# Optimization experiments

Hardware: AMD Instinct MI355X
Metric: run time of the kernel (lower is better)

Reference implementation:

```python
import jax, jax.numpy as jnp
import numpy as np

B, NQ, NKV = 16, 4096, 77
QUERY_DIM, CONTEXT_DIM = 320, 768
HEADS, DIM_HEAD = 8, 64
INNER = HEADS * DIM_HEAD
SCALE = DIM_HEAD ** (-0.5)
MAX_NEG = -jnp.finfo(jnp.float32).max / 2


def setup_inputs() -> dict:
    key = jax.random.key(0)
    ks = jax.random.split(key, 8)
    x = jax.random.normal(ks[0], (B, NQ, QUERY_DIM), dtype=jnp.float32)
    context = jax.random.normal(ks[1], (B, NKV, CONTEXT_DIM), dtype=jnp.float32)
    mask = jax.random.randint(ks[2], (B, 1, 1, NKV), 0, 2).astype(bool)
    s = 0.02
    Wq = jax.random.normal(ks[3], (QUERY_DIM, INNER), dtype=jnp.float32) * s
    Wk = jax.random.normal(ks[4], (CONTEXT_DIM, INNER), dtype=jnp.float32) * s
    Wv = jax.random.normal(ks[5], (CONTEXT_DIM, INNER), dtype=jnp.float32) * s
    Wo = jax.random.normal(ks[6], (INNER, QUERY_DIM), dtype=jnp.float32) * s
    bo = jnp.zeros((QUERY_DIM,), dtype=jnp.float32)
    return {"x": x, "context": context, "mask": mask,
            "Wq": Wq, "Wk": Wk, "Wv": Wv, "Wo": Wo, "bo": bo}


def reference(x, context, mask, Wq, Wk, Wv, Wo, bo):
    # projections (bias-free Linears)
    q = (x @ Wq).reshape(B, NQ, HEADS, DIM_HEAD)        # b q h d
    k = (context @ Wk).reshape(B, NKV, HEADS, DIM_HEAD)  # b k h d
    v = (context @ Wv).reshape(B, NKV, HEADS, DIM_HEAD)  # b k h d
    # additive mask bias: 0 where mask, -finfo.max/2 where ~mask (matches masked_fill_)
    bias = jnp.where(mask, jnp.float32(0), MAX_NEG)      # broadcast to b h q k
    sim = jnp.einsum('bqhd,bkhd->bhqk', q, k) * SCALE + bias
    attn = jax.nn.softmax(sim, axis=-1)
    out = jnp.einsum('bhqk,bkhd->bqhd', attn, v).reshape(B, NQ, INNER)
    return out @ Wo + bo  # dropout p=0 -> identity
```

## Files before the change

### kernel.cpp

```cpp
#include <hip/hip_runtime.h>

typedef unsigned short ushort_t;
typedef __attribute__((ext_vector_type(8))) short bf16x8;
typedef __attribute__((ext_vector_type(4))) float f32x4;

#define B_SZ   16
#define NQ     4096
#define NKV    77
#define QDIM   320
#define CDIM   768
#define HEADS  8
#define DHEAD  64
#define INNER  512
#define M_ROWS (B_SZ * NQ)
#define VT_STR 104

__device__ __forceinline__ ushort_t f2bf(float f) {
  unsigned u = __builtin_bit_cast(unsigned, f);
  u = (u + 0x7fffu + ((u >> 16) & 1u)) >> 16;
  return (ushort_t)u;
}

__device__ __forceinline__ void async16(const ushort_t* g, ushort_t* l) {
  __builtin_amdgcn_global_load_lds(
      (const __attribute__((address_space(1))) unsigned int*)g,
      (__attribute__((address_space(3))) unsigned int*)l,
      16, 0, 0);
}

#define VMCNT(N) asm volatile("s_waitcnt vmcnt(" #N ")" ::: "memory")

#define PREP_X  5242880
#define PREP_T0 (PREP_X + 236544)
#define PREP_T1 (PREP_T0 + 163840)
#define PREP_T2 (PREP_T1 + 786432)
#define PREP_T3 (PREP_T2 + 196608)
__global__ void prep_kernel(const float* __restrict__ x, ushort_t* __restrict__ xb,
                            const float* __restrict__ ctx, ushort_t* __restrict__ cb,
                            const float* __restrict__ Wq, ushort_t* __restrict__ Wqb,
                            const float* __restrict__ Wk, const float* __restrict__ Wv,
                            ushort_t* __restrict__ Wkvb,
                            const float* __restrict__ Wo, ushort_t* __restrict__ Wob,
                            const unsigned char* __restrict__ mraw,
                            float* __restrict__ biasT) {
  if (blockIdx.x == 0) {
    __shared__ int s_u8, s_w4;
    if (threadIdx.x == 0) { s_u8 = 0; s_w4 = 0; }
    __syncthreads();
    const int nbytes = B_SZ * NKV;
    for (int i = threadIdx.x; i < nbytes; i += blockDim.x) {
      unsigned char v = mraw[i];
      if (v && (i & 3)) atomicOr(&s_u8, 1);
      if (v && ((i & 7) == 4)) atomicOr(&s_w4, 1);
    }
    __syncthreads();
    int mode = s_u8 ? 0 : (s_w4 ? 1 : 2);
    for (int i = threadIdx.x; i < B_SZ * 80; i += blockDim.x) {
      int b = i / 80, kv = i - b * 80;
      float bias = -2e30f;
      if (kv < NKV) {
        int idx = b * NKV + kv;
        long long m;
        if (mode == 0)      m = (long long)mraw[idx];
        else if (mode == 1) m = (long long)((const int*)mraw)[idx];
        else                m = ((const long long*)mraw)[idx];
        bias = m ? 0.0f : -1e30f;
      }
      biasT[i] = bias;
    }
  }
  int i = blockIdx.x * blockDim.x + threadIdx.x;
  const int stride = gridDim.x * blockDim.x;
  for (; i < PREP_T3; i += stride) {
    if (i < PREP_X) {
      float4 v = ((const float4*)x)[i];
      ushort4 o;
      o.x = f2bf(v.x); o.y = f2bf(v.y); o.z = f2bf(v.z); o.w = f2bf(v.w);
      ((ushort4*)xb)[i] = o;
    } else if (i < PREP_T0) {
      int j = i - PREP_X;
      float4 v = ((const float4*)ctx)[j];
      ushort4 o;
      o.x = f2bf(v.x); o.y = f2bf(v.y); o.z = f2bf(v.z); o.w = f2bf(v.w);
      ((ushort4*)cb)[j] = o;
    } else if (i < PREP_T1) {
      int j = i - PREP_T0;
      int n = j / QDIM, k = j - n * QDIM;
      Wqb[j] = f2bf(Wq[(size_t)k * INNER + n] * 0.125f);
    } else if (i < PREP_T2) {
      int j = i - PREP_T1;
      int n = j / CDIM, k = j - n * CDIM;
      float v = (n < INNER) ? Wk[(size_t)k * INNER + n]
                            : Wv[(size_t)k * INNER + (n - INNER)];
      Wkvb[j] = f2bf(v);
    } else {
      int j = i - PREP_T2;
      int n = j / INNER, k = j - n * INNER;
      Wob[j] = (n < QDIM) ? f2bf(Wo[(size_t)k * QDIM + n]) : (ushort_t)0;
    }
  }
}

__global__ __launch_bounds__(256) void gemm_bf16(
    const ushort_t* __restrict__ A, const ushort_t* __restrict__ Bt,
    ushort_t* __restrict__ Cb,
    int K, int Astride, int Bstride, int Cstride) {
  __shared__ ushort_t As[128 * 64];
  __shared__ ushort_t Bs[128 * 64];
  const int tid = threadIdx.x;
  const int wid = tid >> 6, lane = tid & 63;
  const int wr = wid >> 1, wc = wid & 1;
  const int tileM = blockIdx.x * 128, tileN = blockIdx.y * 128;

  f32x4 acc[4][4];
#pragma unroll
  for (int m = 0; m < 4; ++m)
#pragma unroll
    for (int n = 0; n < 4; ++n) acc[m][n] = (f32x4){0.f, 0.f, 0.f, 0.f};

  const int srow = lane >> 3;
  const int scol = (lane & 7) * 8;

  for (int kt = 0; kt < K; kt += 64) {
    __syncthreads();
#pragma unroll
    for (int j = 0; j < 4; ++j) {
      int s = wid * 4 + j;
      const ushort_t* ga = A + (size_t)(tileM + s * 8 + srow) * Astride + kt + scol;
      const ushort_t* gb = Bt + (size_t)(tileN + s * 8 + srow) * Bstride + kt + scol;
      async16(ga, As + s * 512);
      async16(gb, Bs + s * 512);
    }
    __syncthreads();
#pragma unroll
    for (int kc = 0; kc < 2; ++kc) {
      bf16x8 af[4], bfr[4];
#pragma unroll
      for (int m = 0; m < 4; ++m)
        af[m] = *(const bf16x8*)&As[(wr * 64 + m * 16 + (lane & 15)) * 64 + kc * 32 + (lane >> 4) * 8];
#pragma unroll
      for (int n = 0; n < 4; ++n)
        bfr[n] = *(const bf16x8*)&Bs[(wc * 64 + n * 16 + (lane & 15)) * 64 + kc * 32 + (lane >> 4) * 8];
#pragma unroll
      for (int m = 0; m < 4; ++m)
#pragma unroll
        for (int n = 0; n < 4; ++n)
          acc[m][n] = __builtin_amdgcn_mfma_f32_16x16x32_bf16(af[m], bfr[n], acc[m][n], 0, 0, 0);
    }
  }

  const int r0 = tileM + wr * 64;
  const int c0 = tileN + wc * 64;
  const int rl2 = (lane >> 4) * 4;
  const int cl = lane & 15;
#pragma unroll
  for (int m = 0; m < 4; ++m)
#pragma unroll
    for (int n = 0; n < 4; ++n) {
      int col = c0 + n * 16 + cl;
#pragma unroll
      for (int r = 0; r < 4; ++r)
        Cb[(size_t)(r0 + m * 16 + rl2 + r) * Cstride + col] = f2bf(acc[m][n][r]);
    }
}

__global__ void vtrans_kernel(const ushort_t* __restrict__ kvb,
                              ushort_t* __restrict__ vt) {
  const int h = blockIdx.y, b = blockIdx.z;
  const int wid = threadIdx.x >> 6, lane = threadIdx.x & 63;
  const int d = blockIdx.x * 4 + wid;
  ushort_t* dst = vt + (size_t)(b * HEADS + h) * (64 * VT_STR) + d * VT_STR;
  for (int kv = lane; kv < VT_STR; kv += 64)
    dst[kv] = (kv < NKV)
        ? kvb[(size_t)(b * NKV + kv) * 1024 + 512 + h * 64 + d]
        : (ushort_t)0;
}

__global__ __launch_bounds__(512, 2) void gemm_qproj_o(
    const ushort_t* __restrict__ A, const ushort_t* __restrict__ Wt,
    ushort_t* __restrict__ qb) {
  extern __shared__ char sm[];
  const int tid = threadIdx.x, wid = tid >> 6, lane = tid & 63;
  const int rl = lane & 15, g = lane >> 4;
  const int wr = wid & 1, wc = wid >> 1;
  const size_t Mbase = (size_t)blockIdx.x * 128;

  size_t asrc; unsigned adst;
  {
    int c = tid, row = c >> 2, c16 = c & 3;
    asrc = (Mbase + row) * 640 + (unsigned)((c16 * 16) ^ ((row & 3) << 4));
    adst = c * 16;
  }
  size_t bsrc[4]; unsigned bdst[4];
#pragma unroll
  for (int i = 0; i < 4; ++i) {
    int c = tid + i * 512, row = c >> 2, c16 = c & 3;
    bsrc[i] = (size_t)row * 640 + (unsigned)((c16 * 16) ^ ((row & 3) << 4));
    bdst[i] = 8192 + c * 16;
  }
  const char* AB = (const char*)A;
  const char* WtB = (const char*)Wt;

  f32x4 acc[4][8];
#pragma unroll
  for (int m = 0; m < 4; ++m)
#pragma unroll
    for (int n = 0; n < 8; ++n) acc[m][n] = (f32x4){0.f, 0.f, 0.f, 0.f};

#define QSTAGE2(K)                                                          \
  {                                                                         \
    char* bb = sm + (unsigned)((K) % 3) * 40960u;                           \
    async16((const ushort_t*)(AB + asrc + (size_t)(K) * 64),                \
            (ushort_t*)(bb + adst));                                        \
    _Pragma("unroll")                                                       \
    for (int i = 0; i < 4; ++i)                                             \
      async16((const ushort_t*)(WtB + bsrc[i] + (size_t)(K) * 64),          \
              (ushort_t*)(bb + bdst[i]));                                   \
  }

  QSTAGE2(0)
  QSTAGE2(1)
  for (int s = 0; s < 10; ++s) {
    if (s < 8) QSTAGE2(s + 2)
    if (s < 8)       { VMCNT(10); }
    else if (s == 8) { VMCNT(5); }
    else             { VMCNT(0); }
    __builtin_amdgcn_sched_barrier(0);
    __builtin_amdgcn_s_barrier();
    __builtin_amdgcn_sched_barrier(0);

    const char* Ab = sm + (unsigned)(s % 3) * 40960u;
    const char* Bb = Ab + 8192;
    bf16x8 af[4], bfr[8];
#pragma unroll
    for (int m = 0; m < 4; ++m) {
      const int row = wr * 64 + m * 16 + rl;
      af[m] = *(const bf16x8*)(Ab + row * 64 + ((g * 16) ^ ((row & 3) << 4)));
    }
#pragma unroll
    for (int n = 0; n < 8; ++n) {
      const int row = wc * 128 + n * 16 + rl;
      bfr[n] = *(const bf16x8*)(Bb + row * 64 + ((g * 16) ^ ((row & 3) << 4)));
    }
#pragma unroll
    for (int m = 0; m < 4; ++m)
#pragma unroll
      for (int n = 0; n < 8; ++n)
        acc[m][n] = __builtin_amdgcn_mfma_f32_16x16x32_bf16(af[m], bfr[n], acc[m][n], 0, 0, 0);
    __builtin_amdgcn_sched_barrier(0);
    __builtin_amdgcn_s_barrier();
    __builtin_amdgcn_sched_barrier(0);
  }

  ushort_t* eb = (ushort_t*)sm;
#pragma unroll
  for (int h = 0; h < 2; ++h) {
    if (h) __syncthreads();
    if (wr == h) {
#pragma unroll
      for (int m = 0; m < 4; ++m)
#pragma unroll
        for (int n = 0; n < 8; ++n)
#pragma unroll
          for (int r = 0; r < 4; ++r)
            eb[(m * 16 + g * 4 + r) * 512 + wc * 128 + n * 16 + rl] = f2bf(acc[m][n][r]);
    }
    __syncthreads();
#pragma unroll
    for (int i = 0; i < 8; ++i) {
      int c = tid + i * 512, row = c >> 6;
      *(bf16x8*)(qb + (Mbase + h * 64 + row) * 512 + (c & 63) * 8) =
          *(const bf16x8*)(eb + c * 8);
    }
  }
}

__global__ __launch_bounds__(512, 2) void gemm_oproj_p(
    const ushort_t* __restrict__ A, const ushort_t* __restrict__ Wt,
    const float* __restrict__ bo, float* __restrict__ out) {
  extern __shared__ char sm[];
  const int tid = threadIdx.x, wid = tid >> 6, lane = tid & 63;
  const int rl = lane & 15, g = lane >> 4;
  const int wr = wid & 1, wc = wid >> 1;
  const size_t Mbase = (size_t)blockIdx.x * 128;

  size_t asrc; unsigned adst;
  {
    int c = tid, row = c >> 2, c16 = c & 3;
    asrc = (Mbase + row) * 1024 + (unsigned)((c16 * 16) ^ ((row & 3) << 4));
    adst = c * 16;
  }
  size_t bsrc[3]; unsigned bdst[3];
#pragma unroll
  for (int i = 0; i < 3; ++i) {
    int c = tid + i * 512, row = c >> 2, c16 = c & 3;
    bsrc[i] = (size_t)row * 1024 + (unsigned)((c16 * 16) ^ ((row & 3) << 4));
    bdst[i] = 8192 + c * 16;
  }
  const char* AB = (const char*)A;
  const char* WtB = (const char*)Wt;

  f32x4 acc[4][6];
#pragma unroll
  for (int m = 0; m < 4; ++m)
#pragma unroll
    for (int n = 0; n < 6; ++n) acc[m][n] = (f32x4){0.f, 0.f, 0.f, 0.f};

#define OSTAGE(K)                                                           \
  {                                                                         \
    char* bb = sm + (unsigned)((K) % 3) * 32768u;                           \
    async16((const ushort_t*)(AB + asrc + (size_t)(K) * 64),                \
            (ushort_t*)(bb + adst));                                        \
    _Pragma("unroll")                                                       \
    for (int i = 0; i < 3; ++i)                                             \
      async16((const ushort_t*)(WtB + bsrc[i] + (size_t)(K) * 64),          \
              (ushort_t*)(bb + bdst[i]));                                   \
  }

  OSTAGE(0)
  OSTAGE(1)
  for (int s = 0; s < 16; ++s) {
    if (s < 14) OSTAGE(s + 2)
    if (s < 14)       { VMCNT(8); }
    else if (s == 14) { VMCNT(4); }
    else              { VMCNT(0); }
    __builtin_amdgcn_sched_barrier(0);
    __builtin_amdgcn_s_barrier();
    __builtin_amdgcn_sched_barrier(0);

    const char* Ab = sm + (unsigned)(s % 3) * 32768u;
    const char* Bb = Ab + 8192;
    bf16x8 af[4], bfr[6];
#pragma unroll
    for (int m = 0; m < 4; ++m) {
      const int row = wr * 64 + m * 16 + rl;
      af[m] = *(const bf16x8*)(Ab + row * 64 + ((g * 16) ^ ((row & 3) << 4)));
    }
#pragma unroll
    for (int n = 0; n < 6; ++n) {
      const int row = wc * 96 + n * 16 + rl;
      bfr[n] = *(const bf16x8*)(Bb + row * 64 + ((g * 16) ^ ((row & 3) << 4)));
    }
#pragma unroll
    for (int m = 0; m < 4; ++m)
#pragma unroll
      for (int n = 0; n < 6; ++n)
        acc[m][n] = __builtin_amdgcn_mfma_f32_16x16x32_bf16(af[m], bfr[n], acc[m][n], 0, 0, 0);
    __builtin_amdgcn_sched_barrier(0);
    __builtin_amdgcn_s_barrier();
    __builtin_amdgcn_sched_barrier(0);
  }

  const size_t r0 = Mbase + wr * 64;
  const int c0 = wc * 96;
#pragma unroll
  for (int n = 0; n < 6; ++n) {
    int col = c0 + n * 16 + rl;
    if (col < QDIM) {
      float bv = bo[col];
#pragma unroll
      for (int m = 0; m < 4; ++m)
#pragma unroll
        for (int r = 0; r < 4; ++r)
          out[(r0 + m * 16 + g * 4 + r) * QDIM + col] = acc[m][n][r] + bv;
    }
  }
}

__global__ __launch_bounds__(256) void attn_kernel(
    const ushort_t* __restrict__ qb, const ushort_t* __restrict__ kvb,
    const ushort_t* __restrict__ vt, const float* __restrict__ biasT,
    ushort_t* __restrict__ ab) {
  __shared__ ushort_t Vt[64 * VT_STR];
  __shared__ ushort_t P[4 * 16 * VT_STR];
  const int qt = blockIdx.x, h = blockIdx.y, b = blockIdx.z;
  const int tid = threadIdx.x, wid = tid >> 6, lane = tid & 63;
  const int rl = lane & 15;
  const int kh = (lane >> 4) * 8;

  const ushort_t* vtg = vt + (size_t)(b * HEADS + h) * (64 * VT_STR);
  for (int i = tid; i < 832; i += 256) async16(vtg + i * 8, Vt + i * 8);
  for (int i = tid; i < 832; i += 256)
    *(bf16x8*)&P[i * 8] = (bf16x8){0, 0, 0, 0, 0, 0, 0, 0};

  bf16x8 kf[5][2];
  float bias_v[5];
#pragma unroll
  for (int nt = 0; nt < 5; ++nt) {
    int kv = nt * 16 + rl;
    bias_v[nt] = biasT[b * 80 + kv];
    kf[nt][0] = (bf16x8){0, 0, 0, 0, 0, 0, 0, 0};
    kf[nt][1] = (bf16x8){0, 0, 0, 0, 0, 0, 0, 0};
    if (kv < NKV) {
      const ushort_t* kp = &kvb[(size_t)(b * NKV + kv) * 1024 + h * 64 + kh];
      kf[nt][0] = *(const bf16x8*)kp;
      kf[nt][1] = *(const bf16x8*)(kp + 32);
    }
  }
  __syncthreads();

  const int qbase = b * NQ + qt * 256;
  const int pbase = wid * (16 * VT_STR);
#pragma unroll 1
  for (int chunk = 0; chunk < 4; ++chunk) {
    if (chunk) __syncthreads();
    const int row0 = chunk * 64 + wid * 16;

    const ushort_t* qp = &qb[(size_t)(qbase + row0 + rl) * INNER + h * 64 + kh];
    bf16x8 qf0 = *(const bf16x8*)qp;
    bf16x8 qf1 = *(const bf16x8*)(qp + 32);

    f32x4 s[5];
#pragma unroll
    for (int nt = 0; nt < 5; ++nt) {
      s[nt] = (f32x4){0.f, 0.f, 0.f, 0.f};
      s[nt] = __builtin_amdgcn_mfma_f32_16x16x32_bf16(qf0, kf[nt][0], s[nt], 0, 0, 0);
      s[nt] = __builtin_amdgcn_mfma_f32_16x16x32_bf16(qf1, kf[nt][1], s[nt], 0, 0, 0);
    }

    float mx[4] = {-3.0e38f, -3.0e38f, -3.0e38f, -3.0e38f};
#pragma unroll
    for (int nt = 0; nt < 5; ++nt)
#pragma unroll
      for (int r = 0; r < 4; ++r) {
        float v = s[nt][r] + bias_v[nt];
        s[nt][r] = v;
        mx[r] = fmaxf(mx[r], v);
      }
#pragma unroll
    for (int d = 1; d < 16; d <<= 1)
#pragma unroll
      for (int r = 0; r < 4; ++r) mx[r] = fmaxf(mx[r], __shfl_xor(mx[r], d, 64));

    float sm_[4] = {0.f, 0.f, 0.f, 0.f};
#pragma unroll
    for (int nt = 0; nt < 5; ++nt)
#pragma unroll
      for (int r = 0; r < 4; ++r) {
        float p = __expf(s[nt][r] - mx[r]);
        s[nt][r] = p;
        sm_[r] += p;
      }
#pragma unroll
    for (int d = 1; d < 16; d <<= 1)
#pragma unroll
      for (int r = 0; r < 4; ++r) sm_[r] += __shfl_xor(sm_[r], d, 64);

    float rcp[4];
#pragma unroll
    for (int r = 0; r < 4; ++r) rcp[r] = 1.0f / sm_[r];

#pragma unroll
    for (int nt = 0; nt < 5; ++nt)
#pragma unroll
      for (int r = 0; r < 4; ++r)
        P[pbase + ((lane >> 4) * 4 + r) * VT_STR + nt * 16 + rl] = f2bf(s[nt][r]);

    f32x4 o[4];
#pragma unroll
    for (int n = 0; n < 4; ++n) o[n] = (f32x4){0.f, 0.f, 0.f, 0.f};
#pragma unroll
    for (int kc = 0; kc < 3; ++kc) {
      bf16x8 pf = *(const bf16x8*)&P[pbase + rl * VT_STR + kc * 32 + kh];
#pragma unroll
      for (int n = 0; n < 4; ++n) {
        bf16x8 vf = *(const bf16x8*)&Vt[(n * 16 + rl) * VT_STR + kc * 32 + kh];
        o[n] = __builtin_amdgcn_mfma_f32_16x16x32_bf16(pf, vf, o[n], 0, 0, 0);
      }
    }

#pragma unroll
    for (int n = 0; n < 4; ++n)
#pragma unroll
      for (int r = 0; r < 4; ++r)
        P[pbase + ((lane >> 4) * 4 + r) * VT_STR + n * 16 + rl] = f2bf(o[n][r] * rcp[r]);

    __syncthreads();

    {
      const int rflat = tid >> 2, d0 = (tid & 3) * 16;
      const ushort_t* src = &P[(rflat >> 4) * (16 * VT_STR) + (rflat & 15) * VT_STR + d0];
      ushort_t* dst = &ab[(size_t)(qbase + chunk * 64 + rflat) * INNER + h * 64 + d0];
      *(bf16x8*)dst = *(const bf16x8*)src;
      *(bf16x8*)(dst + 8) = *(const bf16x8*)(src + 8);
    }
  }
}

extern "C" void kernel_launch(void* const* d_in, const int* in_sizes, int n_in,
                              void* d_out, int out_size, void* d_ws, size_t ws_size,
                              hipStream_t stream) {
  (void)in_sizes; (void)n_in; (void)out_size; (void)ws_size;
  const float* x   = (const float*)d_in[0];
  const float* ctx = (const float*)d_in[1];
  const unsigned char* mask = (const unsigned char*)d_in[2];
  const float* Wq = (const float*)d_in[3];
  const float* Wk = (const float*)d_in[4];
  const float* Wv = (const float*)d_in[5];
  const float* Wo = (const float*)d_in[6];
  const float* bo = (const float*)d_in[7];
  float* out = (float*)d_out;

  hipFuncSetAttribute((const void*)gemm_qproj_o,
                      hipFuncAttributeMaxDynamicSharedMemorySize, 122880);
  hipFuncSetAttribute((const void*)gemm_oproj_p,
                      hipFuncAttributeMaxDynamicSharedMemorySize, 98304);

  char* ws = (char*)d_ws;
  size_t off = 0;
  auto alloc = [&](size_t bytes) {
    char* p = ws + off;
    off += (bytes + 255) & ~(size_t)255;
    return p;
  };
  float*    biasT = (float*)alloc(B_SZ * 80 * sizeof(float));
  ushort_t* ab    = (ushort_t*)alloc((size_t)M_ROWS * INNER * 2);
  ushort_t* qb    = (ushort_t*)alloc((size_t)M_ROWS * INNER * 2);
  ushort_t* xb    = (ushort_t*)alloc((size_t)M_ROWS * QDIM * 2);
  ushort_t* cb    = (ushort_t*)alloc((size_t)1280 * CDIM * 2);
  ushort_t* Wqb   = (ushort_t*)alloc((size_t)INNER * QDIM * 2);
  ushort_t* Wkvb  = (ushort_t*)alloc((size_t)1024 * CDIM * 2);
  ushort_t* Wob   = (ushort_t*)alloc((size_t)384 * INNER * 2);
  ushort_t* kvb   = (ushort_t*)alloc((size_t)1280 * 1024 * 2);
  ushort_t* vt    = (ushort_t*)alloc((size_t)B_SZ * HEADS * 64 * VT_STR * 2);

  prep_kernel<<<2048, 256, 0, stream>>>(x, xb, ctx, cb, Wq, Wqb,
                                        Wk, Wv, Wkvb, Wo, Wob, mask, biasT);

  gemm_qproj_o<<<M_ROWS / 128, 512, 122880, stream>>>(xb, Wqb, qb);
  dim3 g2(1280 / 128, 1024 / 128);
  gemm_bf16<<<g2, 256, 0, stream>>>(cb, Wkvb, kvb, CDIM, CDIM, CDIM, 1024);
  vtrans_kernel<<<dim3(16, HEADS, B_SZ), 256, 0, stream>>>(kvb, vt);
  attn_kernel<<<dim3(NQ / 256, HEADS, B_SZ), 256, 0, stream>>>(qb, kvb, vt, biasT, ab);
  gemm_oproj_p<<<M_ROWS / 128, 512, 98304, stream>>>(ab, Wob, bo, out);
}
```

Baseline: 189.5 us.

## Split Q-projection along N and double-buffer O-projection to raise occupancy

The Q-projection GEMM now tiles 128x256 instead of 128x512, launching a 2D grid of twice as many blocks. This halves the accumulators and the LDS per stage so the launch bound allows 4 blocks per CU. The epilogue uses a padded 272-element row stride. The O-projection GEMM drops from a 3-stage to a 2-stage LDS ring, issuing the next load after the trailing barrier, which cuts LDS to 64KB for higher occupancy at the cost of less prefetch depth.

```diff
diff --git a/kernel.cpp b/kernel.cpp
--- a/kernel.cpp
+++ b/kernel.cpp
@@ -176,7 +176,7 @@
         : (ushort_t)0;
 }
 
-__global__ __launch_bounds__(512, 2) void gemm_qproj_o(
+__global__ __launch_bounds__(512, 4) void gemm_qproj_ns(
     const ushort_t* __restrict__ A, const ushort_t* __restrict__ Wt,
     ushort_t* __restrict__ qb) {
   extern __shared__ char sm[];
@@ -184,6 +184,7 @@
   const int rl = lane & 15, g = lane >> 4;
   const int wr = wid & 1, wc = wid >> 1;
   const size_t Mbase = (size_t)blockIdx.x * 128;
+  const int Nbase = blockIdx.y * 256;
 
   size_t asrc; unsigned adst;
   {
@@ -191,61 +192,61 @@
     asrc = (Mbase + row) * 640 + (unsigned)((c16 * 16) ^ ((row & 3) << 4));
     adst = c * 16;
   }
-  size_t bsrc[4]; unsigned bdst[4];
-#pragma unroll
-  for (int i = 0; i < 4; ++i) {
+  size_t bsrc[2]; unsigned bdst[2];
+#pragma unroll
+  for (int i = 0; i < 2; ++i) {
     int c = tid + i * 512, row = c >> 2, c16 = c & 3;
-    bsrc[i] = (size_t)row * 640 + (unsigned)((c16 * 16) ^ ((row & 3) << 4));
+    bsrc[i] = (size_t)(Nbase + row) * 640 + (unsigned)((c16 * 16) ^ ((row & 3) << 4));
     bdst[i] = 8192 + c * 16;
   }
   const char* AB = (const char*)A;
   const char* WtB = (const char*)Wt;
 
-  f32x4 acc[4][8];
+  f32x4 acc[4][4];
 #pragma unroll
   for (int m = 0; m < 4; ++m)
 #pragma unroll
-    for (int n = 0; n < 8; ++n) acc[m][n] = (f32x4){0.f, 0.f, 0.f, 0.f};
-
-#define QSTAGE2(K)                                                          \
+    for (int n = 0; n < 4; ++n) acc[m][n] = (f32x4){0.f, 0.f, 0.f, 0.f};
+
+#define QSTG(K)                                                             \
   {                                                                         \
-    char* bb = sm + (unsigned)((K) % 3) * 40960u;                           \
+    char* bb = sm + (unsigned)((K) % 3) * 24576u;                           \
     async16((const ushort_t*)(AB + asrc + (size_t)(K) * 64),                \
             (ushort_t*)(bb + adst));                                        \
     _Pragma("unroll")                                                       \
-    for (int i = 0; i < 4; ++i)                                             \
+    for (int i = 0; i < 2; ++i)                                             \
       async16((const ushort_t*)(WtB + bsrc[i] + (size_t)(K) * 64),          \
               (ushort_t*)(bb + bdst[i]));                                   \
   }
 
-  QSTAGE2(0)
-  QSTAGE2(1)
+  QSTG(0)
+  QSTG(1)
   for (int s = 0; s < 10; ++s) {
-    if (s < 8) QSTAGE2(s + 2)
-    if (s < 8)       { VMCNT(10); }
-    else if (s == 8) { VMCNT(5); }
+    if (s < 8) QSTG(s + 2)
+    if (s < 8)       { VMCNT(6); }
+    else if (s == 8) { VMCNT(3); }
     else             { VMCNT(0); }
     __builtin_amdgcn_sched_barrier(0);
     __builtin_amdgcn_s_barrier();
     __builtin_amdgcn_sched_barrier(0);
 
-    const char* Ab = sm + (unsigned)(s % 3) * 40960u;
+    const char* Ab = sm + (unsigned)(s % 3) * 24576u;
     const char* Bb = Ab + 8192;
-    bf16x8 af[4], bfr[8];
+    bf16x8 af[4], bfr[4];
 #pragma unroll
     for (int m = 0; m < 4; ++m) {
       const int row = wr * 64 + m * 16 + rl;
       af[m] = *(const bf16x8*)(Ab + row * 64 + ((g * 16) ^ ((row & 3) << 4)));
     }
 #pragma unroll
-    for (int n = 0; n < 8; ++n) {
-      const int row = wc * 128 + n * 16 + rl;
+    for (int n = 0; n < 4; ++n) {
+      const int row = wc * 64 + n * 16 + rl;
       bfr[n] = *(const bf16x8*)(Bb + row * 64 + ((g * 16) ^ ((row & 3) << 4)));
     }
 #pragma unroll
     for (int m = 0; m < 4; ++m)
 #pragma unroll
-      for (int n = 0; n < 8; ++n)
+      for (int n = 0; n < 4; ++n)
         acc[m][n] = __builtin_amdgcn_mfma_f32_16x16x32_bf16(af[m], bfr[n], acc[m][n], 0, 0, 0);
     __builtin_amdgcn_sched_barrier(0);
     __builtin_amdgcn_s_barrier();
@@ -255,27 +256,27 @@
   ushort_t* eb = (ushort_t*)sm;
 #pragma unroll
   for (int h = 0; h < 2; ++h) {
-    if (h) __syncthreads();
+    __syncthreads();
     if (wr == h) {
 #pragma unroll
       for (int m = 0; m < 4; ++m)
 #pragma unroll
-        for (int n = 0; n < 8; ++n)
+        for (int n = 0; n < 4; ++n)
 #pragma unroll
           for (int r = 0; r < 4; ++r)
-            eb[(m * 16 + g * 4 + r) * 512 + wc * 128 + n * 16 + rl] = f2bf(acc[m][n][r]);
-    }
-    __syncthreads();
-#pragma unroll
-    for (int i = 0; i < 8; ++i) {
-      int c = tid + i * 512, row = c >> 6;
-      *(bf16x8*)(qb + (Mbase + h * 64 + row) * 512 + (c & 63) * 8) =
-          *(const bf16x8*)(eb + c * 8);
-    }
-  }
-}
-
-__global__ __launch_bounds__(512, 2) void gemm_oproj_p(
+            eb[(m * 16 + g * 4 + r) * 272 + wc * 64 + n * 16 + rl] = f2bf(acc[m][n][r]);
+    }
+    __syncthreads();
+#pragma unroll
+    for (int i = 0; i < 4; ++i) {
+      int c = tid + i * 512, row = c >> 5, c8 = c & 31;
+      *(bf16x8*)(qb + (Mbase + h * 64 + row) * 512 + Nbase + c8 * 8) =
+          *(const bf16x8*)(eb + row * 272 + c8 * 8);
+    }
+  }
+}
+
+__global__ __launch_bounds__(512, 4) void gemm_oproj_p2(
     const ushort_t* __restrict__ A, const ushort_t* __restrict__ Wt,
     const float* __restrict__ bo, float* __restrict__ out) {
   extern __shared__ char sm[];
@@ -306,9 +307,9 @@
 #pragma unroll
     for (int n = 0; n < 6; ++n) acc[m][n] = (f32x4){0.f, 0.f, 0.f, 0.f};
 
-#define OSTAGE(K)                                                           \
+#define OSTG2(K)                                                            \
   {                                                                         \
-    char* bb = sm + (unsigned)((K) % 3) * 32768u;                           \
+    char* bb = sm + (unsigned)((K) & 1) * 32768u;                           \
     async16((const ushort_t*)(AB + asrc + (size_t)(K) * 64),                \
             (ushort_t*)(bb + adst));                                        \
     _Pragma("unroll")                                                       \
@@ -317,18 +318,16 @@
               (ushort_t*)(bb + bdst[i]));                                   \
   }
 
-  OSTAGE(0)
-  OSTAGE(1)
+  OSTG2(0)
+  OSTG2(1)
   for (int s = 0; s < 16; ++s) {
-    if (s < 14) OSTAGE(s + 2)
-    if (s < 14)       { VMCNT(8); }
-    else if (s == 14) { VMCNT(4); }
-    else              { VMCNT(0); }
+    if (s < 15)      { VMCNT(4); }
+    else             { VMCNT(0); }
     __builtin_amdgcn_sched_barrier(0);
     __builtin_amdgcn_s_barrier();
     __builtin_amdgcn_sched_barrier(0);
 
-    const char* Ab = sm + (unsigned)(s % 3) * 32768u;
+    const char* Ab = sm + (unsigned)(s & 1) * 32768u;
     const char* Bb = Ab + 8192;
     bf16x8 af[4], bfr[6];
 #pragma unroll
@@ -349,6 +348,7 @@
     __builtin_amdgcn_sched_barrier(0);
     __builtin_amdgcn_s_barrier();
     __builtin_amdgcn_sched_barrier(0);
+    if (s < 14) OSTG2(s + 2)
   }
 
   const size_t r0 = Mbase + wr * 64;
@@ -501,10 +501,10 @@
   const float* bo = (const float*)d_in[7];
   float* out = (float*)d_out;
 
-  hipFuncSetAttribute((const void*)gemm_qproj_o,
-                      hipFuncAttributeMaxDynamicSharedMemorySize, 122880);
-  hipFuncSetAttribute((const void*)gemm_oproj_p,
-                      hipFuncAttributeMaxDynamicSharedMemorySize, 98304);
+  hipFuncSetAttribute((const void*)gemm_qproj_ns,
+                      hipFuncAttributeMaxDynamicSharedMemorySize, 73728);
+  hipFuncSetAttribute((const void*)gemm_oproj_p2,
+                      hipFuncAttributeMaxDynamicSharedMemorySize, 65536);
 
   char* ws = (char*)d_ws;
   size_t off = 0;
@@ -527,10 +527,10 @@
   prep_kernel<<<2048, 256, 0, stream>>>(x, xb, ctx, cb, Wq, Wqb,
                                         Wk, Wv, Wkvb, Wo, Wob, mask, biasT);
 
-  gemm_qproj_o<<<M_ROWS / 128, 512, 122880, stream>>>(xb, Wqb, qb);
+  gemm_qproj_ns<<<dim3(512, 2), 512, 73728, stream>>>(xb, Wqb, qb);
   dim3 g2(1280 / 128, 1024 / 128);
   gemm_bf16<<<g2, 256, 0, stream>>>(cb, Wkvb, kvb, CDIM, CDIM, CDIM, 1024);
   vtrans_kernel<<<dim3(16, HEADS, B_SZ), 256, 0, stream>>>(kvb, vt);
   attn_kernel<<<dim3(NQ / 256, HEADS, B_SZ), 256, 0, stream>>>(qb, kvb, vt, biasT, ab);
-  gemm_oproj_p<<<M_ROWS / 128, 512, 98304, stream>>>(ab, Wob, bo, out);
-}
+  gemm_oproj_p2<<<M_ROWS / 128, 512, 65536, stream>>>(ab, Wob, bo, out);
+}
```

Result: slower. 237.9 us (+25.5%).
